# Kernel optimization log

Measured on AMD Instinct MI355X. Metric: run time of the kernel, lower is better.

The kernel has to match this reference:

```python
import jax, jax.numpy as jnp
import numpy as np
import math

SEQ, BATCH, HID, HEADS = 2048, 2, 2048, 16
HEAD_DIM = HID // HEADS
ROPE_BASE = 10000.0


def setup_inputs() -> dict:
    key = jax.random.key(0)
    k1, k2, k3 = jax.random.split(key, 3)
    hidden_states = jax.random.normal(k1, (SEQ, BATCH, HID), dtype=jnp.float32)
    # causal mask: True means masked (gpt2-style attention_mask_func fills with -10000)
    attention_mask = jnp.triu(jnp.ones((SEQ, SEQ), dtype=bool), k=1)[None, None, :, :]
    w_qkv = jax.random.normal(k2, (3 * HID, HID), dtype=jnp.float32) * 0.02
    b_qkv = jnp.zeros((3 * HID,), dtype=jnp.float32)
    w_dense = jax.random.normal(k3, (HID, HID), dtype=jnp.float32) * 0.02
    b_dense = jnp.zeros((HID,), dtype=jnp.float32)
    return {"hidden_states": hidden_states, "attention_mask": attention_mask,
            "w_qkv": w_qkv, "b_qkv": b_qkv, "w_dense": w_dense, "b_dense": b_dense}


def _rotary_cos_sin(seq_len, dim, dtype):
    inv_freq = 1.0 / (ROPE_BASE ** (jnp.arange(0, dim, 2, dtype=jnp.float32) / dim))
    t = jnp.arange(seq_len, dtype=jnp.float32)
    freqs = jnp.einsum("s,d->sd", t, inv_freq)
    emb = jnp.concatenate([freqs, freqs], axis=-1)  # [s, dim]
    # broadcast to [s, 1, 1, dim] over (batch, heads)
    return jnp.cos(emb)[:, None, None, :].astype(dtype), jnp.sin(emb)[:, None, None, :].astype(dtype)


def _rotate_half(x):
    x1, x2 = jnp.split(x, 2, axis=-1)
    return jnp.concatenate([-x2, x1], axis=-1)


def reference(hidden_states, attention_mask, w_qkv, b_qkv, w_dense, b_dense):
    s, b, h = hidden_states.shape
    # QKV projection: [s, b, 3h] -> [s, b, nh, 3*hd] -> split
    mixed = hidden_states @ w_qkv.T + b_qkv
    mixed = mixed.reshape(s, b, HEADS, 3 * HEAD_DIM)
    q, k, v = jnp.split(mixed, 3, axis=-1)  # each [s, b, nh, hd]
    # rotary (rotary_pct == 1 -> full head dim)
    cos, sin = _rotary_cos_sin(s, HEAD_DIM, q.dtype)
    q = q * cos + _rotate_half(q) * sin
    k = k * cos + _rotate_half(k) * sin
    # attention scores [b, nh, s_q, s_k]
    norm_factor = math.sqrt(HEAD_DIM)
    scores = jnp.einsum("sbhd,tbhd->bhst", q, k) / norm_factor
    scores = jnp.where(attention_mask, jnp.asarray(-10000.0, scores.dtype), scores)
    # softmax in fp32
    probs = jax.nn.softmax(scores.astype(jnp.float32), axis=-1).astype(scores.dtype)
    # context [s, b, nh, hd] -> [s, b, h]
    context = jnp.einsum("bhst,tbhd->sbhd", probs, v).reshape(s, b, h)
    # dense with skip_bias_add: bias returned separately
    output = context @ w_dense.T
    return output, b_dense
```

## Files before the change

### kernel.cpp

```cpp
#include <hip/hip_runtime.h>
#include <cstdint>
#include <math.h>


typedef unsigned short u16;
typedef __bf16 bf16x8 __attribute__((ext_vector_type(8)));
typedef float floatx4 __attribute__((ext_vector_type(4)));

#define SEQ 2048
#define BATCH 2
#define HID 2048
#define NH 16
#define HD 128

__device__ __forceinline__ u16 f2bf(float f) {
  union { float f; uint32_t u; } v; v.f = f;
  uint32_t u = v.u;
  return (u16)((u + 0x7FFFu + ((u >> 16) & 1u)) >> 16);
}

__device__ __forceinline__ void st8_bf16(u16* dst, const float* s) {
  uint32_t pk[4];
#pragma unroll
  for (int j = 0; j < 4; j++)
    pk[j] = (uint32_t)f2bf(s[2 * j]) | ((uint32_t)f2bf(s[2 * j + 1]) << 16);
  *(uint4*)dst = make_uint4(pk[0], pk[1], pk[2], pk[3]);
}

__device__ __forceinline__ void gl16(const u16* g, u16* l) {
  __builtin_amdgcn_global_load_lds(
      (const __attribute__((address_space(1))) void*)g,
      (__attribute__((address_space(3))) void*)l, 16, 0, 0);
}

__global__ __launch_bounds__(256) void cvt_inputs(
    const float* __restrict__ W, const float* __restrict__ Hid,
    u16* __restrict__ wb, u16* __restrict__ Ah, u16* __restrict__ wvw,
    const float* __restrict__ bd, float* __restrict__ out) {
  const int blk = blockIdx.x;
  const int c0 = threadIdx.x * 8;
  if (blk == 10240) {
#pragma unroll
    for (int j = 0; j < 8; j++)
      out[(size_t)SEQ * BATCH * HID + c0 + j] = bd[c0 + j];
    return;
  }
  const float* src;
  u16* dst;
  if (blk < 4096) {
    int dt = blk >> 7, r = blk & 127;
    int srow = (dt < 16) ? ((dt * 3 + 1) * 128 + r) : (((dt - 16) * 3) * 128 + r);
    src = W + (size_t)srow * HID;
    dst = wb + (size_t)blk * HID;
  } else if (blk < 8192) {
    int r = blk - 4096;
    src = Hid + (size_t)r * HID;
    dst = Ah + (size_t)r * HID;
  } else {
    int v = blk - 8192;
    int h = v >> 7, r = v & 127;
    src = W + (size_t)((h * 3 + 2) * 128 + r) * HID;
    dst = wvw + (size_t)v * HID;
  }
  float t[8];
  *(floatx4*)&t[0] = *(const floatx4*)(src + c0);
  *(floatx4*)&t[4] = *(const floatx4*)(src + c0 + 4);
  st8_bf16(dst + c0, t);
}

__global__ __launch_bounds__(256) void cvt_wd(const float* __restrict__ W,
                                              u16* __restrict__ wd) {
  const int r = blockIdx.x;
  const int c0 = threadIdx.x * 8;
  float t[8];
  const float* src = W + (size_t)r * HID;
  *(floatx4*)&t[0] = *(const floatx4*)(src + c0);
  *(floatx4*)&t[4] = *(const floatx4*)(src + c0 + 4);
  st8_bf16(wd + (size_t)r * HID + c0, t);
}

__global__ __launch_bounds__(256, 2) void qkv(
    const u16* __restrict__ Ah, const u16* __restrict__ wb,
    const u16* __restrict__ wvw, const float* __restrict__ bias,
    u16* __restrict__ Qw, u16* __restrict__ Kw, u16* __restrict__ Vt) {
  __shared__ __align__(16) u16 As[128 * 64];
  __shared__ __align__(16) u16 Bs[128 * 64];
  const int tid = threadIdx.x;
  const int wv = tid >> 6, lane = tid & 63;
  const int quad = lane >> 4, l16 = lane & 15;
  const int wt = blockIdx.x;
  const bool isv = (wt >= 32);
  const int bm = blockIdx.y;
  const int rowA0 = bm * 128;
  const int wm = (wv >> 1) * 64;
  const int wn = (wv & 1) * 32;
  const int ntoff[4] = {wn, wn + 16, wn + 64, wn + 80};

  const int lrow = wv * 32 + (lane >> 3);
  const int lcol = (lane & 7) * 8;
  const u16* Ag = Ah + (size_t)(rowA0 + lrow) * HID + lcol;
  const u16* Bg = (isv ? wvw + ((size_t)(wt - 32) * 128 + lrow) * HID
                       : wb + ((size_t)wt * 128 + lrow) * HID) + lcol;
  u16* Al = &As[(wv * 32) * 64];
  u16* Bl = &Bs[(wv * 32) * 64];

  floatx4 acc[4][4];
#pragma unroll
  for (int i = 0; i < 4; i++)
#pragma unroll
    for (int j = 0; j < 4; j++) acc[i][j] = (floatx4){0.f, 0.f, 0.f, 0.f};

  for (int kb = 0; kb < HID; kb += 64) {
#pragma unroll
    for (int j = 0; j < 4; j++) {
      gl16(Ag + (size_t)j * 8 * HID + kb, Al + j * 8 * 64);
      gl16(Bg + (size_t)j * 8 * HID + kb, Bl + j * 8 * 64);
    }
    __syncthreads();
#pragma unroll
    for (int ks = 0; ks < 64; ks += 32) {
      bf16x8 af[4], bfr[4];
#pragma unroll
      for (int mi = 0; mi < 4; mi++)
        af[mi] = *(const bf16x8*)&As[(wm + mi * 16 + l16) * 64 + ks + quad * 8];
#pragma unroll
      for (int ni = 0; ni < 4; ni++)
        bfr[ni] = *(const bf16x8*)&Bs[(ntoff[ni] + l16) * 64 + ks + quad * 8];
#pragma unroll
      for (int mi = 0; mi < 4; mi++)
#pragma unroll
        for (int ni = 0; ni < 4; ni++)
          acc[mi][ni] = __builtin_amdgcn_mfma_f32_16x16x32_bf16(
              af[mi], bfr[ni], acc[mi][ni], 0, 0, 0);
    }
    __syncthreads();
  }

  if (!isv) {
    const int seg = (wt < 16) ? 1 : 0;
    const int head = wt & 15;
    u16* dst = seg ? Kw : Qw;
    float bv[4];
#pragma unroll
    for (int ni = 0; ni < 4; ni++)
      bv[ni] = bias[(head * 3 + seg) * 128 + ntoff[ni] + l16];
    const float RC = 0.20762050593045951f;
    const float f0 = exp2f(-(float)(wn + l16) * RC);
    const float f1 = exp2f(-(float)(wn + 16 + l16) * RC);

#pragma unroll
    for (int mi = 0; mi < 4; mi++) {
#pragma unroll
      for (int reg = 0; reg < 4; reg++) {
        int r = rowA0 + wm + mi * 16 + quad * 4 + reg;
        int s = r >> 1, b = r & 1;
        size_t base = ((size_t)(b * NH + head) * SEQ + s) * HD;
        float sv, cv;
        sincosf((float)s * f0, &sv, &cv);
        {
          float lo = acc[mi][0][reg] + bv[0];
          float hi = acc[mi][2][reg] + bv[2];
          dst[base + wn + l16] = f2bf(lo * cv - hi * sv);
          dst[base + wn + l16 + 64] = f2bf(hi * cv + lo * sv);
        }
        sincosf((float)s * f1, &sv, &cv);
        {
          float lo = acc[mi][1][reg] + bv[1];
          float hi = acc[mi][3][reg] + bv[3];
          dst[base + wn + 16 + l16] = f2bf(lo * cv - hi * sv);
          dst[base + wn + 16 + l16 + 64] = f2bf(hi * cv + lo * sv);
        }
      }
    }
  } else {
    const int head = wt - 32;
    float bv[4];
#pragma unroll
    for (int ni = 0; ni < 4; ni++)
      bv[ni] = bias[(head * 3 + 2) * 128 + ntoff[ni] + l16];
#pragma unroll
    for (int mi = 0; mi < 4; mi++) {
#pragma unroll
      for (int ni = 0; ni < 4; ni++) {
        int d = ntoff[ni] + l16;
#pragma unroll
        for (int reg = 0; reg < 4; reg++) {
          int r = rowA0 + wm + mi * 16 + quad * 4 + reg;
          int s = r >> 1, b = r & 1;
          Vt[((size_t)(b * NH + head) * HD + d) * SEQ + s] =
              f2bf(acc[mi][ni][reg] + bv[ni]);
        }
      }
    }
  }
}

__global__ __launch_bounds__(512, 4) void attn(
    const u16* __restrict__ Qw, const u16* __restrict__ Kw,
    const u16* __restrict__ Vt, u16* __restrict__ ctx) {
  __shared__ __align__(16) u16 Ks[64 * 128];
  __shared__ __align__(16) u16 Vs[128 * 64 + 2304];
  __shared__ __align__(16) u16 Pl[8 * 16 * 72];

  const int tid = threadIdx.x;
  const int wv = tid >> 6, lane = tid & 63;
  const int quad = lane >> 4, l16 = lane & 15;

  const int lin = blockIdx.y * gridDim.x + blockIdx.x;
  const int xcdsel = lin & 7;
  const int k = lin >> 3;
  const int bh_hi = k >> 4;
  const int x = k & 15;
  const int bh = (bh_hi << 3) | xcdsel;
  const int qt = ((bh_hi >> 1) & 1) ? (15 - x) : x;

  const int b = bh >> 4, h = bh & 15;
  const int sw = qt * 128 + wv * 16;
  const size_t bhoff = (size_t)bh * SEQ * HD;

  bf16x8 qf[4];
#pragma unroll
  for (int kc = 0; kc < 4; kc++)
    qf[kc] = *(const bf16x8*)&Qw[bhoff + (size_t)(sw + l16) * HD + kc * 32 +
                                 quad * 8];

  floatx4 o[8];
#pragma unroll
  for (int ni = 0; ni < 8; ni++) o[ni] = (floatx4){0.f, 0.f, 0.f, 0.f};
  float mst[4], lst[4];
#pragma unroll
  for (int r = 0; r < 4; r++) { mst[r] = -1e30f; lst[r] = 0.f; }

  const int nt = qt * 2 + 2;
  const float SCL2 = 0.088388347648318447f * 1.442695040888963f;
  const float MSK2 = -10000.0f * 1.442695040888963f;

#define STAGE(tt)                                                              \
  {                                                                            \
    _Pragma("unroll") for (int i = 0; i < 2; i++) {                            \
      int c = i * 512 + tid;                                                   \
      int rk = c >> 4, uk = c & 15;                                            \
      gl16(&Kw[bhoff + (size_t)((tt) * 64 + rk) * HD + (uk ^ (rk & 7)) * 8],   \
           &Ks[(i * 512 + wv * 64) * 8]);                                      \
      int rv_ = c >> 3, uv = c & 7;                                            \
      gl16(&Vt[bhoff + (size_t)rv_ * SEQ + (tt) * 64 + (uv ^ (rv_ & 7)) * 8],  \
           &Vs[(i * 512 + wv * 64) * 8]);                                      \
    }                                                                          \
  }

  for (int t = 0; t < nt; t++) {
    __syncthreads();
    STAGE(t);
    __syncthreads();

    const bool active = (t * 64 <= sw + 15);
    if (active) {
      floatx4 sa[4];
#pragma unroll
      for (int ni = 0; ni < 4; ni++) sa[ni] = (floatx4){0.f, 0.f, 0.f, 0.f};
      __builtin_amdgcn_s_setprio(1);
#pragma unroll
      for (int kc = 0; kc < 4; kc++) {
        bf16x8 kf[4];
#pragma unroll
        for (int ni = 0; ni < 4; ni++)
          kf[ni] = *(const bf16x8*)&Ks[(ni * 16 + l16) * 128 +
                                       (((kc * 4 + quad) ^ (l16 & 7)) * 8)];
#pragma unroll
        for (int ni = 0; ni < 4; ni++)
          sa[ni] = __builtin_amdgcn_mfma_f32_16x16x32_bf16(qf[kc], kf[ni],
                                                           sa[ni], 0, 0, 0);
      }
      __builtin_amdgcn_s_setprio(0);

      float alpha[4];
#pragma unroll
      for (int reg = 0; reg < 4; reg++) {
        const int rr = quad * 4 + reg;
        const int sq = sw + rr;
        float rv[4];
#pragma unroll
        for (int ni = 0; ni < 4; ni++) {
          int sk = t * 64 + ni * 16 + l16;
          float v = sa[ni][reg] * SCL2;
          if (sk > sq) v = MSK2;
          rv[ni] = v;
        }
        float rmax = fmaxf(fmaxf(rv[0], rv[1]), fmaxf(rv[2], rv[3]));
        rmax = fmaxf(rmax, __shfl_xor(rmax, 1));
        rmax = fmaxf(rmax, __shfl_xor(rmax, 2));
        rmax = fmaxf(rmax, __shfl_xor(rmax, 4));
        rmax = fmaxf(rmax, __shfl_xor(rmax, 8));
        float mn = fmaxf(mst[reg], rmax);
        float al = exp2f(mst[reg] - mn);
        float rs = 0.f;
#pragma unroll
        for (int ni = 0; ni < 4; ni++) {
          float p = exp2f(rv[ni] - mn);
          rs += p;
          Pl[wv * 1152 + rr * 72 + ni * 16 + l16] = f2bf(p);
        }
        rs += __shfl_xor(rs, 1);
        rs += __shfl_xor(rs, 2);
        rs += __shfl_xor(rs, 4);
        rs += __shfl_xor(rs, 8);
        lst[reg] = lst[reg] * al + rs;
        mst[reg] = mn;
        alpha[reg] = al;
      }
#pragma unroll
      for (int ni = 0; ni < 8; ni++)
#pragma unroll
        for (int reg = 0; reg < 4; reg++) o[ni][reg] *= alpha[reg];

      __builtin_amdgcn_s_setprio(1);
#pragma unroll
      for (int kc = 0; kc < 2; kc++) {
        bf16x8 pf =
            *(const bf16x8*)&Pl[wv * 1152 + l16 * 72 + kc * 32 + quad * 8];
#pragma unroll
        for (int ni = 0; ni < 8; ni++) {
          bf16x8 vf = *(const bf16x8*)&Vs[(ni * 16 + l16) * 64 +
                                          (((kc * 4 + quad) ^ (l16 & 7)) * 8)];
          o[ni] = __builtin_amdgcn_mfma_f32_16x16x32_bf16(pf, vf, o[ni], 0, 0,
                                                          0);
        }
      }
      __builtin_amdgcn_s_setprio(0);
    }
  }

#pragma unroll
  for (int reg = 0; reg < 4; reg++) {
    float inv = 1.0f / lst[reg];
    int sq = sw + quad * 4 + reg;
    size_t rbase = ((size_t)(sq * BATCH + b)) * HID + h * HD;
#pragma unroll
    for (int ni = 0; ni < 8; ni++)
      ctx[rbase + ni * 16 + l16] = f2bf(o[ni][reg] * inv);
  }
#undef STAGE
}

__global__ __launch_bounds__(256, 2) void dense_gemm(
    const u16* __restrict__ A, const u16* __restrict__ Wd,
    float* __restrict__ out, float* __restrict__ po) {
  __shared__ __align__(16) u16 As[128 * 64];
  __shared__ __align__(16) u16 Bs[128 * 64];
  const int tid = threadIdx.x;
  const int wv = tid >> 6, lane = tid & 63;
  const int quad = lane >> 4, l16 = lane & 15;
  const int bn = blockIdx.x, bm = blockIdx.y;
  const int kz = blockIdx.z;
  const int rowA0 = bm * 128, rowB0 = bn * 128;
  const int wm = (wv >> 1) * 64;
  const int wn = (wv & 1) * 64;
  const int ntoff[4] = {wn, wn + 16, wn + 32, wn + 48};

  const int lrow = wv * 32 + (lane >> 3);
  const int lcol = (lane & 7) * 8;
  const u16* Ag = A + (size_t)(rowA0 + lrow) * HID + lcol;
  const u16* Bg = Wd + (size_t)(rowB0 + lrow) * HID + lcol;
  u16* Al = &As[(wv * 32) * 64];
  u16* Bl = &Bs[(wv * 32) * 64];

  floatx4 acc[4][4];
#pragma unroll
  for (int i = 0; i < 4; i++)
#pragma unroll
    for (int j = 0; j < 4; j++) acc[i][j] = (floatx4){0.f, 0.f, 0.f, 0.f};

  const int kb0 = kz * 1024;
  for (int kb = kb0; kb < kb0 + 1024; kb += 64) {
#pragma unroll
    for (int j = 0; j < 4; j++) {
      gl16(Ag + (size_t)j * 8 * HID + kb, Al + j * 8 * 64);
      gl16(Bg + (size_t)j * 8 * HID + kb, Bl + j * 8 * 64);
    }
    __syncthreads();
#pragma unroll
    for (int ks = 0; ks < 64; ks += 32) {
      bf16x8 af[4], bfr[4];
#pragma unroll
      for (int mi = 0; mi < 4; mi++)
        af[mi] = *(const bf16x8*)&As[(wm + mi * 16 + l16) * 64 + ks + quad * 8];
#pragma unroll
      for (int ni = 0; ni < 4; ni++)
        bfr[ni] = *(const bf16x8*)&Bs[(ntoff[ni] + l16) * 64 + ks + quad * 8];
#pragma unroll
      for (int mi = 0; mi < 4; mi++)
#pragma unroll
        for (int ni = 0; ni < 4; ni++)
          acc[mi][ni] = __builtin_amdgcn_mfma_f32_16x16x32_bf16(
              af[mi], bfr[ni], acc[mi][ni], 0, 0, 0);
    }
    __syncthreads();
  }

  float* dst = kz ? po : out;
#pragma unroll
  for (int mi = 0; mi < 4; mi++)
#pragma unroll
    for (int reg = 0; reg < 4; reg++) {
      int r = rowA0 + wm + mi * 16 + quad * 4 + reg;
#pragma unroll
      for (int ni = 0; ni < 4; ni++)
        dst[(size_t)r * HID + rowB0 + ntoff[ni] + l16] = acc[mi][ni][reg];
    }
}

__global__ __launch_bounds__(256) void combine(float* __restrict__ out,
                                               const float* __restrict__ po) {
  size_t i = ((size_t)blockIdx.x * 256 + threadIdx.x) * 4;
  floatx4 a = *(const floatx4*)(out + i);
  floatx4 c = *(const floatx4*)(po + i);
  *(floatx4*)(out + i) = a + c;
}

extern "C" void kernel_launch(void* const* d_in, const int* in_sizes, int n_in,
                              void* d_out, int out_size, void* d_ws,
                              size_t ws_size, hipStream_t stream) {
  const float *hidden = nullptr, *w_qkv = nullptr, *b_qkv = nullptr;
  const float *w_dense = nullptr, *b_dense = nullptr;
  for (int i = 0; i < n_in; i++) {
    long s = in_sizes[i];
    if (s == 8388608L) hidden = (const float*)d_in[i];
    else if (s == 12582912L) w_qkv = (const float*)d_in[i];
    else if (s == 6144L) b_qkv = (const float*)d_in[i];
    else if (s == 4194304L) w_dense = (const float*)d_in[i];
    else if (s == 2048L) b_dense = (const float*)d_in[i];
  }
  float* out = (float*)d_out;

  char* ws = (char*)d_ws;
  u16* Qw = (u16*)(ws);
  u16* Kw = (u16*)(ws + 16777216ll);
  u16* wb = (u16*)(ws + 33554432ll);
  u16* Ah = (u16*)(ws + 50331648ll);
  u16* ctx = (u16*)(ws + 50331648ll);
  u16* wd = (u16*)(ws);
  float* po = (float*)(ws + 16777216ll);
  u16* wvw = (u16*)d_out;
  u16* Vt = (u16*)d_out + 4194304;

  cvt_inputs<<<dim3(10241), dim3(256), 0, stream>>>(w_qkv, hidden, wb, Ah, wvw,
                                                    b_dense, out);
  qkv<<<dim3(48, 32), dim3(256), 0, stream>>>(Ah, wb, wvw, b_qkv, Qw, Kw, Vt);
  attn<<<dim3(16, 32), dim3(512), 0, stream>>>(Qw, Kw, Vt, ctx);
  cvt_wd<<<dim3(2048), dim3(256), 0, stream>>>(w_dense, wd);
  dense_gemm<<<dim3(16, 32, 2), dim3(256), 0, stream>>>(ctx, wd, out, po);
  combine<<<dim3(8192), dim3(256), 0, stream>>>(out, po);
}
```

Before: 438.6 us.

## Use rotation recurrence for RoPE, native bf16 cast, reorder dense grid

In the QKV epilogue, per-row sincosf calls are replaced by a few initial sincosf values that are advanced by an angle-addition rotation each mi step. This removes most transcendental work but lets rounding error build up across the four steps. The attention softmax now stores P with a native __bf16 cast instead of the manual rounding helper. The dense GEMM grid is reordered so the split-K index varies fastest, which places the two K-halves of a tile next to each other in launch order and may improve cache locality.

After: 425.8 us. -2.9%, faster.

```diff
diff --git a/kernel.cpp b/kernel.cpp
--- a/kernel.cpp
+++ b/kernel.cpp
@@ -31,6 +31,12 @@
   __builtin_amdgcn_global_load_lds(
       (const __attribute__((address_space(1))) void*)g,
       (__attribute__((address_space(3))) void*)l, 16, 0, 0);
+}
+
+__device__ __forceinline__ void rot2(float& c, float& s, float cd, float sd) {
+  float t = c * cd - s * sd;
+  s = s * cd + c * sd;
+  c = t;
 }
 
 __global__ __launch_bounds__(256) void cvt_inputs(
@@ -147,6 +153,16 @@
     const float RC = 0.20762050593045951f;
     const float f0 = exp2f(-(float)(wn + l16) * RC);
     const float f1 = exp2f(-(float)(wn + 16 + l16) * RC);
+    const int S0 = (rowA0 + wm) >> 1;
+    const int q2 = quad * 2;
+    float cA0, sA0, cB0, sB0, c80, s80;
+    float cA1, sA1, cB1, sB1, c81, s81;
+    sincosf((float)(S0 + q2) * f0, &sA0, &cA0);
+    sincosf((float)(S0 + q2 + 1) * f0, &sB0, &cB0);
+    sincosf(8.0f * f0, &s80, &c80);
+    sincosf((float)(S0 + q2) * f1, &sA1, &cA1);
+    sincosf((float)(S0 + q2 + 1) * f1, &sB1, &cB1);
+    sincosf(8.0f * f1, &s81, &c81);
 
 #pragma unroll
     for (int mi = 0; mi < 4; mi++) {
@@ -155,22 +171,27 @@
         int r = rowA0 + wm + mi * 16 + quad * 4 + reg;
         int s = r >> 1, b = r & 1;
         size_t base = ((size_t)(b * NH + head) * SEQ + s) * HD;
-        float sv, cv;
-        sincosf((float)s * f0, &sv, &cv);
+        float cv0 = (reg < 2) ? cA0 : cB0;
+        float sv0 = (reg < 2) ? sA0 : sB0;
+        float cv1 = (reg < 2) ? cA1 : cB1;
+        float sv1 = (reg < 2) ? sA1 : sB1;
         {
           float lo = acc[mi][0][reg] + bv[0];
           float hi = acc[mi][2][reg] + bv[2];
-          dst[base + wn + l16] = f2bf(lo * cv - hi * sv);
-          dst[base + wn + l16 + 64] = f2bf(hi * cv + lo * sv);
-        }
-        sincosf((float)s * f1, &sv, &cv);
+          dst[base + wn + l16] = f2bf(lo * cv0 - hi * sv0);
+          dst[base + wn + l16 + 64] = f2bf(hi * cv0 + lo * sv0);
+        }
         {
           float lo = acc[mi][1][reg] + bv[1];
           float hi = acc[mi][3][reg] + bv[3];
-          dst[base + wn + 16 + l16] = f2bf(lo * cv - hi * sv);
-          dst[base + wn + 16 + l16 + 64] = f2bf(hi * cv + lo * sv);
+          dst[base + wn + 16 + l16] = f2bf(lo * cv1 - hi * sv1);
+          dst[base + wn + 16 + l16 + 64] = f2bf(hi * cv1 + lo * sv1);
         }
       }
+      rot2(cA0, sA0, c80, s80);
+      rot2(cB0, sB0, c80, s80);
+      rot2(cA1, sA1, c81, s81);
+      rot2(cB1, sB1, c81, s81);
     }
   } else {
     const int head = wt - 32;
@@ -298,7 +319,7 @@
         for (int ni = 0; ni < 4; ni++) {
           float p = exp2f(rv[ni] - mn);
           rs += p;
-          Pl[wv * 1152 + rr * 72 + ni * 16 + l16] = f2bf(p);
+          ((__bf16*)Pl)[wv * 1152 + rr * 72 + ni * 16 + l16] = (__bf16)p;
         }
         rs += __shfl_xor(rs, 1);
         rs += __shfl_xor(rs, 2);
@@ -350,8 +371,8 @@
   const int tid = threadIdx.x;
   const int wv = tid >> 6, lane = tid & 63;
   const int quad = lane >> 4, l16 = lane & 15;
-  const int bn = blockIdx.x, bm = blockIdx.y;
-  const int kz = blockIdx.z;
+  const int kz = blockIdx.x;
+  const int bn = blockIdx.y, bm = blockIdx.z;
   const int rowA0 = bm * 128, rowB0 = bn * 128;
   const int wm = (wv >> 1) * 64;
   const int wn = (wv & 1) * 64;
@@ -448,6 +469,6 @@
   qkv<<<dim3(48, 32), dim3(256), 0, stream>>>(Ah, wb, wvw, b_qkv, Qw, Kw, Vt);
   attn<<<dim3(16, 32), dim3(512), 0, stream>>>(Qw, Kw, Vt, ctx);
   cvt_wd<<<dim3(2048), dim3(256), 0, stream>>>(w_dense, wd);
-  dense_gemm<<<dim3(16, 32, 2), dim3(256), 0, stream>>>(ctx, wd, out, po);
+  dense_gemm<<<dim3(2, 16, 32), dim3(256), 0, stream>>>(ctx, wd, out, po);
   combine<<<dim3(8192), dim3(256), 0, stream>>>(out, po);
 }
```
